# Performance work log

Measured on AMD Instinct MI355X. Metric: run time of the kernel, lower is better.

The kernel has to match this reference:

```python
import jax, jax.numpy as jnp
import numpy as np

PI = 3.14159  # module uses this truncated pi
CX, CY, FOCAL = 256.0, 256.0, 608.365


def _sh_basis(depth):
    # depth: [B, H, W] (already rescaled to (d+1)/2)
    B, H, W = depth.shape
    gx = jnp.arange(W, dtype=depth.dtype)
    gy = jnp.arange(H, dtype=depth.dtype)
    xx, yy = jnp.meshgrid(gx, gy)            # 'xy' indexing, matches np.meshgrid
    xx = (xx - CX) / FOCAL * depth           # [B,H,W]
    yy = (yy - CY) / FOCAL * depth
    p = jnp.stack([xx, yy, depth], axis=-1)  # [B,H,W,3]

    p_ctr = p[:, 1:-1, 1:-1]
    vw = p_ctr - p[:, 1:-1, 2:]
    vs = p[:, 2:, 1:-1] - p_ctr
    ve = p_ctr - p[:, 1:-1, :-2]
    vn = p[:, :-2, 1:-1] - p_ctr
    normal = jnp.cross(vw, vs) + jnp.cross(ve, vn)     # [B,H-2,W-2,3]
    nmag = jnp.sqrt(jnp.sum(normal * normal, axis=-1)) # [B,H-2,W-2]
    nunit = normal / nmag[..., None]

    pad3 = ((0, 0), (1, 1), (1, 1), (0, 0))
    pad2 = ((0, 0), (1, 1), (1, 1))
    n_raw = jnp.pad(normal, pad3)   # UNNORMALIZED normals (faithful to source: normal_*_pad)
    n_u = jnp.pad(nunit, pad3)      # normalized normals (n_x/n_y/n_z)
    mag = jnp.pad(nmag, pad2)

    nx, ny, nz = n_u[..., 0], n_u[..., 1], n_u[..., 2]
    x2, y2, z2 = nx * nx, ny * ny, nz * nz
    xy, xz, yz = nx * ny, nx * nz, ny * nz

    c0 = PI * np.sqrt(1.0 / (4 * PI))
    c1 = 2 * PI / 3.0 * np.sqrt(3.0 / (4 * PI))
    c2 = PI / 4.0 * 0.5 * np.sqrt(5.0 / (4 * PI))
    c3 = PI / 4.0 * 3.0 * np.sqrt(5.0 / (12 * PI))
    c4 = PI / 4.0 * 3.0 * np.sqrt(5.0 / (48 * PI))

    N = jnp.stack([
        c0 * mag,
        c1 * n_raw[..., 2],
        c1 * n_raw[..., 0],
        c1 * n_raw[..., 1],
        c2 * (2 * z2 - x2 - y2) * mag,
        c3 * xz * mag,
        c3 * yz * mag,
        c4 * (x2 - y2) * mag,
        c3 * xy * mag,
    ], axis=-1)  # [B,H,W,9]
    return N


def setup_inputs() -> dict:
    key = jax.random.key(0)
    k1, k2, k3 = jax.random.split(key, 3)
    B, H, W = 8, 512, 512
    input_img = jax.random.normal(k1, (B, 3, H, W), dtype=jnp.float32)
    depth_target = jax.random.uniform(k2, (B, 1, H, W), dtype=jnp.float32)
    albedo = jax.random.uniform(k3, (B, 3, H, W), dtype=jnp.float32)
    return {"input_img": input_img, "depth_target": depth_target, "albedo": albedo}


def reference(input_img, depth_target, albedo):
    B, C, H, W = input_img.shape
    P = H * W
    depth = (depth_target + 1.0) / 2.0           # [B,1,H,W]
    img = (input_img + 1.0) / 2.0                # [B,3,H,W]
    # mask: binary, 1 wherever channel-0 of scaled image is nonzero
    mask = (img[:, :1] != 0).astype(img.dtype)   # [B,1,H,W]
    img = img * mask

    N = _sh_basis(depth[:, 0])                   # [B,H,W,9]
    A_fla = N.reshape(B, P, 9)

    rhoc_mask = (albedo * mask).reshape(B, 3, P)
    # Faithful bug reproduction: the source loop overwrites rhoc_N each channel
    # iteration, so only the LAST channel (index 2) of rhoc_mask is used for all
    # three least-squares systems.
    A = A_fla * rhoc_mask[:, 2, :, None]         # [B,P,9]
    b = img.reshape(B, 3, P)                     # [B,3,P]

    # Masked least squares: rows with mask==0 have A-row==0 and b==0, so solving
    # over all P rows via normal equations equals torch.gels over nonzero rows.
    AtA = jnp.einsum('bpi,bpj->bij', A, A)       # [B,9,9]
    Atb = jnp.einsum('bcp,bpi->bci', b, A)       # [B,3,9]
    S = jnp.linalg.solve(AtA[:, None], Atb[..., None])[..., 0]  # [B,3,9]
    return S
```

## Files before the change

### kernel.cpp

```cpp
#include <hip/hip_runtime.h>
#include <math.h>

#define HH 512
#define WW 512
#define NB 8
#define ROWS_PER_BLOCK 8
#define NACC 72

__global__ __launch_bounds__(256, 2)
void accum_kernel(const float* __restrict__ img,
                  const float* __restrict__ dep,
                  const float* __restrict__ alb,
                  float* __restrict__ ws)
{
    const int b   = blockIdx.y;
    const int y0  = blockIdx.x * ROWS_PER_BLOCK;
    const int tid = threadIdx.x;

    const float c0 = (float)(3.14159 * sqrt(1.0 / (4.0 * 3.14159)));
    const float c1 = (float)(2.0 * 3.14159 / 3.0 * sqrt(3.0 / (4.0 * 3.14159)));
    const float c2 = (float)(3.14159 / 4.0 * 0.5 * sqrt(5.0 / (4.0 * 3.14159)));
    const float c3 = (float)(3.14159 / 4.0 * 3.0 * sqrt(5.0 / (12.0 * 3.14159)));
    const float c4 = (float)(3.14159 / 4.0 * 3.0 * sqrt(5.0 / (48.0 * 3.14159)));

    float acc[NACC];
#pragma unroll
    for (int i = 0; i < NACC; ++i) acc[i] = 0.0f;

    const float* depb  = dep + (size_t)b * HH * WW;
    const float* img0b = img + (size_t)(b * 3 + 0) * HH * WW;
    const float* img1b = img + (size_t)(b * 3 + 1) * HH * WW;
    const float* img2b = img + (size_t)(b * 3 + 2) * HH * WW;
    const float* alb2b = alb + (size_t)(b * 3 + 2) * HH * WW;

    for (int r = 0; r < ROWS_PER_BLOCK; ++r) {
        const int y = y0 + r;
        if (y < 1 || y >= HH - 1) continue;
        const float fy  = ((float)y       - 256.0f) / 608.365f;
        const float fyd = ((float)(y + 1) - 256.0f) / 608.365f;
        const float fyu = ((float)(y - 1) - 256.0f) / 608.365f;
        for (int xi = 0; xi < 2; ++xi) {
            const int x = 1 + tid + xi * 256;
            if (x >= WW - 1) continue;
            const int idx = y * WW + x;

            const float dc = (depb[idx]      + 1.0f) * 0.5f;
            const float dr = (depb[idx + 1]  + 1.0f) * 0.5f;
            const float dl = (depb[idx - 1]  + 1.0f) * 0.5f;
            const float dd = (depb[idx + WW] + 1.0f) * 0.5f;
            const float du = (depb[idx - WW] + 1.0f) * 0.5f;

            const float fx  = ((float)x       - 256.0f) / 608.365f;
            const float fxr = ((float)(x + 1) - 256.0f) / 608.365f;
            const float fxl = ((float)(x - 1) - 256.0f) / 608.365f;

            const float pcx = fx  * dc, pcy = fy  * dc;
            const float prx = fxr * dr, pry = fy  * dr;
            const float plx = fxl * dl, ply = fy  * dl;
            const float pdx = fx  * dd, pdy = fyd * dd;
            const float pux = fx  * du, puy = fyu * du;

            const float vwx = pcx - prx, vwy = pcy - pry, vwz = dc - dr;
            const float vsx = pdx - pcx, vsy = pdy - pcy, vsz = dd - dc;
            const float vex = pcx - plx, vey = pcy - ply, vez = dc - dl;
            const float vnx = pux - pcx, vny = puy - pcy, vnz = du - dc;

            const float nx = (vwy * vsz - vwz * vsy) + (vey * vnz - vez * vny);
            const float ny = (vwz * vsx - vwx * vsz) + (vez * vnx - vex * vnz);
            const float nz = (vwx * vsy - vwy * vsx) + (vex * vny - vey * vnx);

            const float nn   = nx * nx + ny * ny + nz * nz;
            const float mag  = sqrtf(nn);
            const float invm = 1.0f / mag;
            const float uxn = nx * invm, uyn = ny * invm, uzn = nz * invm;
            const float x2 = uxn * uxn, y2 = uyn * uyn, z2 = uzn * uzn;

            const float N0 = c0 * mag;
            const float N1 = c1 * nz;
            const float N2 = c1 * nx;
            const float N3 = c1 * ny;
            const float N4 = c2 * (2.0f * z2 - x2 - y2) * mag;
            const float N5 = c3 * (uxn * uzn) * mag;
            const float N6 = c3 * (uyn * uzn) * mag;
            const float N7 = c4 * (x2 - y2) * mag;
            const float N8 = c3 * (uxn * uyn) * mag;

            const float i0 = (img0b[idx] + 1.0f) * 0.5f;
            const float i1 = (img1b[idx] + 1.0f) * 0.5f;
            const float i2 = (img2b[idx] + 1.0f) * 0.5f;
            const float m  = (i0 != 0.0f) ? 1.0f : 0.0f;
            const float b0 = i0 * m, b1 = i1 * m, b2 = i2 * m;
            const float rho = alb2b[idx] * m;

            float A[9] = {N0 * rho, N1 * rho, N2 * rho, N3 * rho, N4 * rho,
                          N5 * rho, N6 * rho, N7 * rho, N8 * rho};

            int k = 0;
#pragma unroll
            for (int i = 0; i < 9; ++i) {
#pragma unroll
                for (int j = i; j < 9; ++j) {
                    acc[k] = fmaf(A[i], A[j], acc[k]);
                    ++k;
                }
            }
#pragma unroll
            for (int i = 0; i < 9; ++i) {
                acc[45 + i] = fmaf(b0, A[i], acc[45 + i]);
                acc[54 + i] = fmaf(b1, A[i], acc[54 + i]);
                acc[63 + i] = fmaf(b2, A[i], acc[63 + i]);
            }
        }
    }

#pragma unroll
    for (int i = 0; i < NACC; ++i) {
        float v = acc[i];
        v += __shfl_xor(v, 32, 64);
        v += __shfl_xor(v, 16, 64);
        v += __shfl_xor(v, 8, 64);
        v += __shfl_xor(v, 4, 64);
        v += __shfl_xor(v, 2, 64);
        v += __shfl_xor(v, 1, 64);
        acc[i] = v;
    }

    __shared__ float red[4][NACC];
    const int wave = tid >> 6;
    const int lane = tid & 63;
    if (lane == 0) {
#pragma unroll
        for (int i = 0; i < NACC; ++i) red[wave][i] = acc[i];
    }
    __syncthreads();
    if (tid < NACC) {
        const float s = red[0][tid] + red[1][tid] + red[2][tid] + red[3][tid];
        atomicAdd(&ws[b * NACC + tid], s);
    }
}

__global__ void solve_kernel(const float* __restrict__ ws, float* __restrict__ out)
{
    __shared__ float M[NB][9][12];
    const int b = threadIdx.x;
    if (b >= NB) return;

    const float* w = ws + b * NACC;
    int k = 0;
    for (int i = 0; i < 9; ++i) {
        for (int j = i; j < 9; ++j) {
            M[b][i][j] = w[k];
            M[b][j][i] = w[k];
            ++k;
        }
    }
    for (int c = 0; c < 3; ++c)
        for (int i = 0; i < 9; ++i)
            M[b][i][9 + c] = w[45 + c * 9 + i];

    for (int kk = 0; kk < 9; ++kk) {
        int piv = kk;
        float best = fabsf(M[b][kk][kk]);
        for (int i = kk + 1; i < 9; ++i) {
            const float v = fabsf(M[b][i][kk]);
            if (v > best) { best = v; piv = i; }
        }
        if (piv != kk) {
            for (int j = 0; j < 12; ++j) {
                const float t = M[b][kk][j];
                M[b][kk][j] = M[b][piv][j];
                M[b][piv][j] = t;
            }
        }
        const float inv = 1.0f / M[b][kk][kk];
        for (int i = kk + 1; i < 9; ++i) {
            const float f = M[b][i][kk] * inv;
            for (int j = kk; j < 12; ++j)
                M[b][i][j] -= f * M[b][kk][j];
        }
    }
    for (int c = 0; c < 3; ++c) {
        float sol[9];
        for (int kk = 8; kk >= 0; --kk) {
            float v = M[b][kk][9 + c];
            for (int j = kk + 1; j < 9; ++j) v -= M[b][kk][j] * sol[j];
            sol[kk] = v / M[b][kk][kk];
        }
        for (int kk = 0; kk < 9; ++kk)
            out[(b * 3 + c) * 9 + kk] = sol[kk];
    }
}

extern "C" void kernel_launch(void* const* d_in, const int* in_sizes, int n_in,
                              void* d_out, int out_size, void* d_ws, size_t ws_size,
                              hipStream_t stream) {
    const float* img = (const float*)d_in[0];
    const float* dep = (const float*)d_in[1];
    const float* alb = (const float*)d_in[2];
    float* out = (float*)d_out;
    float* ws  = (float*)d_ws;

    hipMemsetAsync(ws, 0, NB * NACC * sizeof(float), stream);

    dim3 grid(HH / ROWS_PER_BLOCK, NB);
    accum_kernel<<<grid, 256, 0, stream>>>(img, dep, alb, ws);
    solve_kernel<<<1, 64, 0, stream>>>(ws, out);
}
```

Before: 112.0 us.

## Vectorize pixel loads with float4 and replace atomics with per-chunk partial sums

Each thread now handles four adjacent pixels per row using float4 loads for depth, image and albedo, and gets its left and right neighbours from registers instead of separate scalar loads. A validity mask zeroes the image-border pixels. Per-block partial sums are written to distinct workspace slots instead of being atomically added, which removes the memset. The solve kernel now runs one block per batch element and reduces the 64 partials before solving. The aim is fewer load instructions and no memset launch, at the cost of more registers per thread and extra reduction work in the solve kernel.

Result: no change. 112.8 us (+0.7%).

```diff
diff --git a/kernel.cpp b/kernel.cpp
--- a/kernel.cpp
+++ b/kernel.cpp
@@ -4,8 +4,8 @@
 #define HH 512
 #define WW 512
 #define NB 8
-#define ROWS_PER_BLOCK 8
 #define NACC 72
+#define CHUNKS 64
 
 __global__ __launch_bounds__(256, 2)
 void accum_kernel(const float* __restrict__ img,
@@ -14,8 +14,11 @@
                   float* __restrict__ ws)
 {
     const int b   = blockIdx.y;
-    const int y0  = blockIdx.x * ROWS_PER_BLOCK;
     const int tid = threadIdx.x;
+    const int tx  = tid & 127;
+    const int ty  = tid >> 7;
+    const int y0  = blockIdx.x * 8;
+    const int x0  = tx * 4;
 
     const float c0 = (float)(3.14159 * sqrt(1.0 / (4.0 * 3.14159)));
     const float c1 = (float)(2.0 * 3.14159 / 3.0 * sqrt(3.0 / (4.0 * 3.14159)));
@@ -33,26 +36,56 @@
     const float* img2b = img + (size_t)(b * 3 + 2) * HH * WW;
     const float* alb2b = alb + (size_t)(b * 3 + 2) * HH * WW;
 
-    for (int r = 0; r < ROWS_PER_BLOCK; ++r) {
-        const int y = y0 + r;
+    float fxv[6];
+#pragma unroll
+    for (int k = 0; k < 6; ++k)
+        fxv[k] = ((float)(x0 - 1 + k) - 256.0f) / 608.365f;
+
+    for (int pass = 0; pass < 4; ++pass) {
+        const int y = y0 + pass * 2 + ty;
         if (y < 1 || y >= HH - 1) continue;
+
+        const int row = y * WW + x0;
         const float fy  = ((float)y       - 256.0f) / 608.365f;
         const float fyd = ((float)(y + 1) - 256.0f) / 608.365f;
         const float fyu = ((float)(y - 1) - 256.0f) / 608.365f;
-        for (int xi = 0; xi < 2; ++xi) {
-            const int x = 1 + tid + xi * 256;
-            if (x >= WW - 1) continue;
-            const int idx = y * WW + x;
-
-            const float dc = (depb[idx]      + 1.0f) * 0.5f;
-            const float dr = (depb[idx + 1]  + 1.0f) * 0.5f;
-            const float dl = (depb[idx - 1]  + 1.0f) * 0.5f;
-            const float dd = (depb[idx + WW] + 1.0f) * 0.5f;
-            const float du = (depb[idx - WW] + 1.0f) * 0.5f;
-
-            const float fx  = ((float)x       - 256.0f) / 608.365f;
-            const float fxr = ((float)(x + 1) - 256.0f) / 608.365f;
-            const float fxl = ((float)(x - 1) - 256.0f) / 608.365f;
+
+        const float4 cen4 = *reinterpret_cast<const float4*>(depb + row);
+        const float4 up4  = *reinterpret_cast<const float4*>(depb + row - WW);
+        const float4 dn4  = *reinterpret_cast<const float4*>(depb + row + WW);
+        const float  lsc  = depb[row - (tx == 0 ? 0 : 1)];
+        const float  rsc  = depb[row + 4];
+        const float4 i04  = *reinterpret_cast<const float4*>(img0b + row);
+        const float4 i14  = *reinterpret_cast<const float4*>(img1b + row);
+        const float4 i24  = *reinterpret_cast<const float4*>(img2b + row);
+        const float4 al4  = *reinterpret_cast<const float4*>(alb2b + row);
+
+        float cA[4] = {(cen4.x + 1.0f) * 0.5f, (cen4.y + 1.0f) * 0.5f,
+                       (cen4.z + 1.0f) * 0.5f, (cen4.w + 1.0f) * 0.5f};
+        float uA[4] = {(up4.x + 1.0f) * 0.5f, (up4.y + 1.0f) * 0.5f,
+                       (up4.z + 1.0f) * 0.5f, (up4.w + 1.0f) * 0.5f};
+        float dA[4] = {(dn4.x + 1.0f) * 0.5f, (dn4.y + 1.0f) * 0.5f,
+                       (dn4.z + 1.0f) * 0.5f, (dn4.w + 1.0f) * 0.5f};
+        const float lT = (lsc + 1.0f) * 0.5f;
+        const float rT = (rsc + 1.0f) * 0.5f;
+        float g0[4] = {i04.x, i04.y, i04.z, i04.w};
+        float g1[4] = {i14.x, i14.y, i14.z, i14.w};
+        float g2[4] = {i24.x, i24.y, i24.z, i24.w};
+        float aA[4] = {al4.x, al4.y, al4.z, al4.w};
+
+#pragma unroll
+        for (int p = 0; p < 4; ++p) {
+            const bool valid = !((p == 0 && tx == 0) || (p == 3 && tx == 127));
+
+            const float dc = cA[p];
+            const float dl = (p == 0) ? lT : cA[(p == 0) ? 0 : p - 1];
+            const float dr = (p == 3) ? rT : cA[(p == 3) ? 3 : p + 1];
+            const float du = uA[p];
+            const float dd = dA[p];
+
+            const float fx  = fxv[p + 1];
+            const float fxl = fxv[p];
+            const float fxr = fxv[p + 2];
 
             const float pcx = fx  * dc, pcy = fy  * dc;
             const float prx = fxr * dr, pry = fy  * dr;
@@ -71,7 +104,8 @@
 
             const float nn   = nx * nx + ny * ny + nz * nz;
             const float mag  = sqrtf(nn);
-            const float invm = 1.0f / mag;
+            const float den  = valid ? mag : 1.0f;
+            const float invm = 1.0f / den;
             const float uxn = nx * invm, uyn = ny * invm, uzn = nz * invm;
             const float x2 = uxn * uxn, y2 = uyn * uyn, z2 = uzn * uzn;
 
@@ -85,25 +119,25 @@
             const float N7 = c4 * (x2 - y2) * mag;
             const float N8 = c3 * (uxn * uyn) * mag;
 
-            const float i0 = (img0b[idx] + 1.0f) * 0.5f;
-            const float i1 = (img1b[idx] + 1.0f) * 0.5f;
-            const float i2 = (img2b[idx] + 1.0f) * 0.5f;
-            const float m  = (i0 != 0.0f) ? 1.0f : 0.0f;
+            const float vf = valid ? 1.0f : 0.0f;
+            const float i0 = (g0[p] + 1.0f) * 0.5f;
+            const float i1 = (g1[p] + 1.0f) * 0.5f;
+            const float i2 = (g2[p] + 1.0f) * 0.5f;
+            const float m  = ((i0 != 0.0f) ? 1.0f : 0.0f) * vf;
             const float b0 = i0 * m, b1 = i1 * m, b2 = i2 * m;
-            const float rho = alb2b[idx] * m;
-
-            float A[9] = {N0 * rho, N1 * rho, N2 * rho, N3 * rho, N4 * rho,
-                          N5 * rho, N6 * rho, N7 * rho, N8 * rho};
+            const float rho = aA[p] * m;
+
+            const float A[9] = {N0 * rho, N1 * rho, N2 * rho, N3 * rho,
+                                N4 * rho, N5 * rho, N6 * rho, N7 * rho, N8 * rho};
 
             int k = 0;
 #pragma unroll
-            for (int i = 0; i < 9; ++i) {
+            for (int i = 0; i < 9; ++i)
 #pragma unroll
                 for (int j = i; j < 9; ++j) {
                     acc[k] = fmaf(A[i], A[j], acc[k]);
                     ++k;
                 }
-            }
 #pragma unroll
             for (int i = 0; i < 9; ++i) {
                 acc[45 + i] = fmaf(b0, A[i], acc[45 + i]);
@@ -135,59 +169,67 @@
     __syncthreads();
     if (tid < NACC) {
         const float s = red[0][tid] + red[1][tid] + red[2][tid] + red[3][tid];
-        atomicAdd(&ws[b * NACC + tid], s);
+        ws[((size_t)b * CHUNKS + blockIdx.x) * NACC + tid] = s;
     }
 }
 
 __global__ void solve_kernel(const float* __restrict__ ws, float* __restrict__ out)
 {
-    __shared__ float M[NB][9][12];
-    const int b = threadIdx.x;
-    if (b >= NB) return;
-
-    const float* w = ws + b * NACC;
-    int k = 0;
-    for (int i = 0; i < 9; ++i) {
-        for (int j = i; j < 9; ++j) {
-            M[b][i][j] = w[k];
-            M[b][j][i] = w[k];
-            ++k;
+    __shared__ float sums[NACC];
+    __shared__ float M[9][12];
+    const int b = blockIdx.x;
+    const int t = threadIdx.x;
+
+    if (t < NACC) {
+        float s = 0.0f;
+        for (int c = 0; c < CHUNKS; ++c)
+            s += ws[((size_t)b * CHUNKS + c) * NACC + t];
+        sums[t] = s;
+    }
+    __syncthreads();
+
+    if (t == 0) {
+        int k = 0;
+        for (int i = 0; i < 9; ++i)
+            for (int j = i; j < 9; ++j) {
+                M[i][j] = sums[k];
+                M[j][i] = sums[k];
+                ++k;
+            }
+        for (int c = 0; c < 3; ++c)
+            for (int i = 0; i < 9; ++i)
+                M[i][9 + c] = sums[45 + c * 9 + i];
+
+        for (int kk = 0; kk < 9; ++kk) {
+            int piv = kk;
+            float best = fabsf(M[kk][kk]);
+            for (int i = kk + 1; i < 9; ++i) {
+                const float v = fabsf(M[i][kk]);
+                if (v > best) { best = v; piv = i; }
+            }
+            if (piv != kk)
+                for (int j = 0; j < 12; ++j) {
+                    const float tmp = M[kk][j];
+                    M[kk][j] = M[piv][j];
+                    M[piv][j] = tmp;
+                }
+            const float inv = 1.0f / M[kk][kk];
+            for (int i = kk + 1; i < 9; ++i) {
+                const float f = M[i][kk] * inv;
+                for (int j = kk; j < 12; ++j)
+                    M[i][j] -= f * M[kk][j];
+            }
         }
-    }
-    for (int c = 0; c < 3; ++c)
-        for (int i = 0; i < 9; ++i)
-            M[b][i][9 + c] = w[45 + c * 9 + i];
-
-    for (int kk = 0; kk < 9; ++kk) {
-        int piv = kk;
-        float best = fabsf(M[b][kk][kk]);
-        for (int i = kk + 1; i < 9; ++i) {
-            const float v = fabsf(M[b][i][kk]);
-            if (v > best) { best = v; piv = i; }
+        for (int c = 0; c < 3; ++c) {
+            float sol[9];
+            for (int kk = 8; kk >= 0; --kk) {
+                float v = M[kk][9 + c];
+                for (int j = kk + 1; j < 9; ++j) v -= M[kk][j] * sol[j];
+                sol[kk] = v / M[kk][kk];
+            }
+            for (int kk = 0; kk < 9; ++kk)
+                out[(b * 3 + c) * 9 + kk] = sol[kk];
         }
-        if (piv != kk) {
-            for (int j = 0; j < 12; ++j) {
-                const float t = M[b][kk][j];
-                M[b][kk][j] = M[b][piv][j];
-                M[b][piv][j] = t;
-            }
-        }
-        const float inv = 1.0f / M[b][kk][kk];
-        for (int i = kk + 1; i < 9; ++i) {
-            const float f = M[b][i][kk] * inv;
-            for (int j = kk; j < 12; ++j)
-                M[b][i][j] -= f * M[b][kk][j];
-        }
-    }
-    for (int c = 0; c < 3; ++c) {
-        float sol[9];
-        for (int kk = 8; kk >= 0; --kk) {
-            float v = M[b][kk][9 + c];
-            for (int j = kk + 1; j < 9; ++j) v -= M[b][kk][j] * sol[j];
-            sol[kk] = v / M[b][kk][kk];
-        }
-        for (int kk = 0; kk < 9; ++kk)
-            out[(b * 3 + c) * 9 + kk] = sol[kk];
     }
 }
 
@@ -200,9 +242,7 @@
     float* out = (float*)d_out;
     float* ws  = (float*)d_ws;
 
-    hipMemsetAsync(ws, 0, NB * NACC * sizeof(float), stream);
-
-    dim3 grid(HH / ROWS_PER_BLOCK, NB);
+    dim3 grid(CHUNKS, NB);
     accum_kernel<<<grid, 256, 0, stream>>>(img, dep, alb, ws);
-    solve_kernel<<<1, 64, 0, stream>>>(ws, out);
+    solve_kernel<<<NB, 128, 0, stream>>>(ws, out);
 }
```
